# Optimization experiments

Measured on AMD Instinct MI355X. Metric: run time of the kernel, lower is better.

## Reference

```python
import jax, jax.numpy as jnp
import numpy as np

IN_FEATURES = 4096
OUT_FEATURES = 4096
MIN_PREC = 3   # min(precisions)
MAXMEM = 6
BL, BH = 4, 5  # floor/ceil of p = sigmoid(0)*3 + 3 = 4.5 (static, matches p.item() usage)


def dequant_kbit(qweight, lut, b):
    """Bitplane LUT dequant: qweight (P, O, IN//32) int32, lut (O, 2**b) -> (O, IN) float.
    Plane j holds one bit per weight (32 weights packed per int32, LSB-first within
    the int32); the first b planes form the b-bit code, plane 0 being the MSB."""
    planes = qweight[:b]                                   # (b, O, IN//32)
    shifts = jnp.arange(32, dtype=jnp.int32)               # bit position within int32
    bits = (planes[..., None] >> shifts) & 1               # (b, O, IN//32, 32)
    bits = bits.reshape(b, planes.shape[1], -1)            # (b, O, IN)
    weights = (jnp.arange(b, dtype=jnp.int32)[::-1])[:, None, None]  # MSB-first
    code = jnp.sum(bits << weights, axis=0)                # (O, IN) int32 in [0, 2**b)
    return jnp.take_along_axis(lut, code, axis=1)          # (O, IN)


def setup_inputs() -> dict:
    key = jax.random.key(0)
    k_x, k_q, k_l4, k_l5, k_b = jax.random.split(key, 5)
    x = jax.random.normal(k_x, (4, 2048, IN_FEATURES), dtype=jnp.float32)
    z = jnp.float32(0.0)  # z_inv = log(z_init/(1-z_init)) with z_init=0.5
    qweight = jax.random.randint(k_q, (MAXMEM, OUT_FEATURES, IN_FEATURES // 32),
                                 minval=-(2**31), maxval=2**31 - 1, dtype=jnp.int32)
    # LUTs: sorted quantization levels per output row (realistic for quantized linear)
    lut4 = jnp.sort(0.02 * jax.random.normal(k_l4, (OUT_FEATURES, 2**BL), dtype=jnp.float32), axis=-1)
    lut5 = jnp.sort(0.02 * jax.random.normal(k_l5, (OUT_FEATURES, 2**BH), dtype=jnp.float32), axis=-1)
    bias = 0.01 * jax.random.normal(k_b, (OUT_FEATURES,), dtype=jnp.float32)
    return {"x": x, "z": z, "lut4": lut4, "lut5": lut5, "bias": bias, "qweight": qweight}


def reference(x, z, lut4, lut5, bias, qweight):
    prange_len = MAXMEM - MIN_PREC
    p = jax.nn.sigmoid(z) * prange_len + MIN_PREC   # 4.5 at init
    r = 1.0 - (p - BL)                              # blend weight for low-bit branch
    wl = dequant_kbit(qweight, lut4, BL)            # (O, IN)
    wh = dequant_kbit(qweight, lut5, BH)            # (O, IN)
    yl = jnp.einsum('bsi,oi->bso', x, wl)
    yh = jnp.einsum('bsi,oi->bso', x, wh)
    return yl * r + yh * (1.0 - r) + bias
```

## Files before the change

kernel.cpp:

```cpp
#include <hip/hip_runtime.h>
#include <hip/hip_bf16.h>


#define IN_F   4096
#define OUT_F  4096
#define M_DIM  8192

#define CAST_BLOCKS 8192
#define DEQ_BLOCKS  2048

typedef __bf16          bf16x8   __attribute__((ext_vector_type(8)));
typedef float           f32x4    __attribute__((ext_vector_type(4)));
typedef unsigned short  ushortx8 __attribute__((ext_vector_type(8)));

__device__ __forceinline__ unsigned short f32_to_bf16(float f) {
    unsigned int u = __builtin_bit_cast(unsigned int, f);
    u += 0x7fffu + ((u >> 16) & 1u);
    return (unsigned short)(u >> 16);
}

__device__ __forceinline__ void async_load16(const void* g, void* l) {
    __builtin_amdgcn_global_load_lds(
        (const __attribute__((address_space(1))) unsigned int*)g,
        (__attribute__((address_space(3))) unsigned int*)l,
        16, 0, 0);
}

__global__ __launch_bounds__(256) void prologue_kernel(
    const float* __restrict__ x,
    const unsigned int* __restrict__ qw,
    const float* __restrict__ lut4,
    const float* __restrict__ lut5,
    const float* __restrict__ zp,
    unsigned short* __restrict__ xb,
    unsigned short* __restrict__ W)
{
    const int tid = threadIdx.x;

    if (blockIdx.x < CAST_BLOCKS) {
        const size_t i = (size_t)blockIdx.x * 4096 + (size_t)tid * 16;
        const f32x4* src = (const f32x4*)(x + i);
        f32x4 a0 = src[0], a1 = src[1], a2 = src[2], a3 = src[3];
        ushortx8 o0, o1;
        #pragma unroll
        for (int e = 0; e < 4; ++e) {
            o0[e]     = f32_to_bf16(a0[e]);
            o0[4 + e] = f32_to_bf16(a1[e]);
            o1[e]     = f32_to_bf16(a2[e]);
            o1[4 + e] = f32_to_bf16(a3[e]);
        }
        ushortx8* dst = (ushortx8*)(xb + i);
        dst[0] = o0;
        dst[1] = o1;
        return;
    }

    __shared__ float sc[2][32];
    const int bid = blockIdx.x - CAST_BLOCKS;
    const int o0 = bid * 2;

    if (tid < 64) {
        const float z   = zp[0];
        const float sig = 1.0f / (1.0f + __expf(-z));
        const float r   = 2.0f - 3.0f * sig;
        const float ri  = 1.0f - r;
        const int row = tid >> 5;
        const int c   = tid & 31;
        sc[row][c] = r * lut4[(o0 + row) * 16 + (c >> 1)]
                   + ri * lut5[(o0 + row) * 32 + c];
    }
    __syncthreads();

    const int gid = bid * 256 + tid;
    const int lo  = (gid >> 7) & 1;

    const int PS = OUT_F * (IN_F / 32);
    const unsigned int q0 = qw[0 * PS + gid];
    const unsigned int q1 = qw[1 * PS + gid];
    const unsigned int q2 = qw[2 * PS + gid];
    const unsigned int q3 = qw[3 * PS + gid];
    const unsigned int q4 = qw[4 * PS + gid];

    unsigned short outv[32];
    #pragma unroll
    for (int i = 0; i < 32; ++i) {
        const unsigned c5 = (((q0 >> i) & 1u) << 4) | (((q1 >> i) & 1u) << 3) |
                            (((q2 >> i) & 1u) << 2) | (((q3 >> i) & 1u) << 1) |
                             ((q4 >> i) & 1u);
        outv[i] = f32_to_bf16(sc[lo][c5]);
    }

    ushortx8* dst = (ushortx8*)(W + (size_t)gid * 32);
    #pragma unroll
    for (int j = 0; j < 4; ++j) {
        ushortx8 v;
        #pragma unroll
        for (int e = 0; e < 8; ++e) v[e] = outv[j * 8 + e];
        dst[j] = v;
    }
}

__global__ __launch_bounds__(256) void gemm_bt_kernel(
    const unsigned short* __restrict__ A,
    const unsigned short* __restrict__ B,
    const float* __restrict__ bias,
    float* __restrict__ C)
{
    __shared__ unsigned short sA[128 * 32];
    __shared__ unsigned short sB[128 * 32];

    const int tid  = threadIdx.x;
    const int lane = tid & 63;
    const int wave = tid >> 6;
    const int bn = blockIdx.x;
    const int bm = blockIdx.y;

    const int wm  = (wave & 1) << 6;
    const int wn  = (wave >> 1) << 6;
    const int l15 = lane & 15;
    const int q   = lane >> 4;

    const int e0 = tid * 8;
    const int r0 = e0 >> 5;
    const int c0 = e0 & 31;

    const unsigned short* gA0 = A + (size_t)(bm * 128 + r0) * IN_F + c0;
    const unsigned short* gA1 = gA0 + (size_t)64 * IN_F;
    const unsigned short* gB0 = B + (size_t)(bn * 128 + r0) * IN_F + c0;
    const unsigned short* gB1 = gB0 + (size_t)64 * IN_F;
    char* lA0 = (char*)sA + e0 * 2;
    char* lA1 = lA0 + 4096;
    char* lB0 = (char*)sB + e0 * 2;
    char* lB1 = lB0 + 4096;

    f32x4 acc[4][4] = {};

    const int aoff = (wm + l15) * 32 + q * 8;
    const int boff = (wn + l15) * 32 + q * 8;

    for (int k0 = 0; k0 < IN_F; k0 += 32) {
        async_load16(gA0 + k0, lA0);
        async_load16(gA1 + k0, lA1);
        async_load16(gB0 + k0, lB0);
        async_load16(gB1 + k0, lB1);
        __syncthreads();

        bf16x8 af[4], bf[4];
        #pragma unroll
        for (int mi = 0; mi < 4; ++mi)
            af[mi] = *(const bf16x8*)(sA + aoff + mi * 512);
        #pragma unroll
        for (int ni = 0; ni < 4; ++ni)
            bf[ni] = *(const bf16x8*)(sB + boff + ni * 512);

        #pragma unroll
        for (int mi = 0; mi < 4; ++mi)
            #pragma unroll
            for (int ni = 0; ni < 4; ++ni)
                acc[mi][ni] = __builtin_amdgcn_mfma_f32_16x16x32_bf16(
                    af[mi], bf[ni], acc[mi][ni], 0, 0, 0);

        __syncthreads();
    }

    const int col0 = bn * 128 + wn + l15;
    const int row0 = bm * 128 + wm + q * 4;
    #pragma unroll
    for (int ni = 0; ni < 4; ++ni) {
        const int col = col0 + ni * 16;
        const float bv = bias[col];
        #pragma unroll
        for (int mi = 0; mi < 4; ++mi) {
            const int row = row0 + mi * 16;
            #pragma unroll
            for (int r = 0; r < 4; ++r)
                C[(size_t)(row + r) * OUT_F + col] = acc[mi][ni][r] + bv;
        }
    }
}

extern "C" void kernel_launch(void* const* d_in, const int* in_sizes, int n_in,
                              void* d_out, int out_size, void* d_ws, size_t ws_size,
                              hipStream_t stream)
{
    const float*        x    = (const float*)d_in[0];
    const float*        z    = (const float*)d_in[1];
    const float*        lut4 = (const float*)d_in[2];
    const float*        lut5 = (const float*)d_in[3];
    const float*        bias = (const float*)d_in[4];
    const unsigned int* qw   = (const unsigned int*)d_in[5];
    float* out = (float*)d_out;

    unsigned short* xb = (unsigned short*)d_ws;
    unsigned short* wb = xb + (size_t)M_DIM * IN_F;

    prologue_kernel<<<CAST_BLOCKS + DEQ_BLOCKS, 256, 0, stream>>>(
        x, qw, lut4, lut5, z, xb, wb);
    gemm_bt_kernel<<<dim3(OUT_F / 128, M_DIM / 128), 256, 0, stream>>>(xb, wb, bias, out);
}
```

Baseline: 569.0 us.

## Rewrite bf16 GEMM with 256x256 tiles, double-buffered LDS pipeline and swizzle

The GEMM kernel now computes 256x256 output tiles with 512 threads and a K step of 64. A and B tiles are double-buffered in LDS and prefetched with global_load_lds in half-tile stages that overlap the MFMA phases, with explicit barriers, waitcnts and setprio. The LDS layout is XOR-swizzled to avoid bank conflicts, and the block index is remapped for L2 locality. This targets the previous kernel's single-buffered load-then-compute stalls and low reuse per tile, at the cost of 128KB of LDS, heavier register use (128 accumulators per thread), and fragile hand-written synchronization.

```diff
diff --git a/kernel.cpp b/kernel.cpp
--- a/kernel.cpp
+++ b/kernel.cpp
@@ -8,6 +8,8 @@
 
 #define CAST_BLOCKS 8192
 #define DEQ_BLOCKS  2048
+
+#define NT (IN_F / 64)
 
 typedef __bf16          bf16x8   __attribute__((ext_vector_type(8)));
 typedef float           f32x4    __attribute__((ext_vector_type(4)));
@@ -24,6 +26,12 @@
         (const __attribute__((address_space(1))) unsigned int*)g,
         (__attribute__((address_space(3))) unsigned int*)l,
         16, 0, 0);
+}
+
+__device__ __forceinline__ void stage_half(const unsigned short* g0,
+                                           unsigned short* l0) {
+    async_load16(g0, l0);
+    async_load16(g0 + (size_t)64 * IN_F, l0 + 4096);
 }
 
 __global__ __launch_bounds__(256) void prologue_kernel(
@@ -100,81 +108,163 @@
     }
 }
 
-__global__ __launch_bounds__(256) void gemm_bt_kernel(
+
+#define MFMA_BF16 __builtin_amdgcn_mfma_f32_16x16x32_bf16
+
+__device__ __forceinline__ void tile_step(
+    int t,
+    const unsigned short* cA, unsigned short* cB, unsigned short* nA,
+    int tid,
+    const unsigned short* gA0, const unsigned short* gA1,
+    const unsigned short* gB0, const unsigned short* gB1,
+    int aBase, int bBase, int ck0, int ck1,
+    f32x4 (&acc)[8][4])
+{
+    bf16x8 af[4], bf0[4], bf1[4];
+
+    #pragma unroll
+    for (int m = 0; m < 4; ++m)
+        af[m] = *(const bf16x8*)(cA + aBase + m * 1024 + ck0);
+    #pragma unroll
+    for (int n = 0; n < 4; ++n)
+        bf0[n] = *(const bf16x8*)(cB + bBase + n * 1024 + ck0);
+    if (t + 1 < NT) stage_half(gA0 + (size_t)(t + 1) * 64, nA + tid * 8);
+    __builtin_amdgcn_s_barrier();
+    asm volatile("s_waitcnt lgkmcnt(0)" ::: "memory");
+    __builtin_amdgcn_sched_barrier(0);
+    __builtin_amdgcn_s_setprio(1);
+    #pragma unroll
+    for (int m = 0; m < 4; ++m)
+        #pragma unroll
+        for (int n = 0; n < 4; ++n)
+            acc[m][n] = MFMA_BF16(af[m], bf0[n], acc[m][n], 0, 0, 0);
+    __builtin_amdgcn_s_setprio(0);
+    __builtin_amdgcn_sched_barrier(0);
+    __builtin_amdgcn_s_barrier();
+
+    #pragma unroll
+    for (int m = 0; m < 4; ++m)
+        af[m] = *(const bf16x8*)(cA + aBase + m * 1024 + ck1);
+    #pragma unroll
+    for (int n = 0; n < 4; ++n)
+        bf1[n] = *(const bf16x8*)(cB + bBase + n * 1024 + ck1);
+    if (t + 1 < NT) stage_half(gA1 + (size_t)(t + 1) * 64, nA + 8192 + tid * 8);
+    __builtin_amdgcn_s_barrier();
+    asm volatile("s_waitcnt lgkmcnt(0)" ::: "memory");
+    __builtin_amdgcn_sched_barrier(0);
+    __builtin_amdgcn_s_setprio(1);
+    #pragma unroll
+    for (int m = 0; m < 4; ++m)
+        #pragma unroll
+        for (int n = 0; n < 4; ++n)
+            acc[m][n] = MFMA_BF16(af[m], bf1[n], acc[m][n], 0, 0, 0);
+    __builtin_amdgcn_s_setprio(0);
+    __builtin_amdgcn_sched_barrier(0);
+    __builtin_amdgcn_s_barrier();
+
+    #pragma unroll
+    for (int m = 0; m < 4; ++m)
+        af[m] = *(const bf16x8*)(cA + aBase + (m + 4) * 1024 + ck0);
+    if (t + 2 < NT) stage_half(gB0 + (size_t)(t + 2) * 64, cB + tid * 8);
+    __builtin_amdgcn_s_barrier();
+    asm volatile("s_waitcnt lgkmcnt(0)" ::: "memory");
+    __builtin_amdgcn_sched_barrier(0);
+    __builtin_amdgcn_s_setprio(1);
+    #pragma unroll
+    for (int m = 0; m < 4; ++m)
+        #pragma unroll
+        for (int n = 0; n < 4; ++n)
+            acc[m + 4][n] = MFMA_BF16(af[m], bf0[n], acc[m + 4][n], 0, 0, 0);
+    __builtin_amdgcn_s_setprio(0);
+    __builtin_amdgcn_sched_barrier(0);
+    __builtin_amdgcn_s_barrier();
+
+    #pragma unroll
+    for (int m = 0; m < 4; ++m)
+        af[m] = *(const bf16x8*)(cA + aBase + (m + 4) * 1024 + ck1);
+    if (t + 2 < NT) stage_half(gB1 + (size_t)(t + 2) * 64, cB + 8192 + tid * 8);
+    if (t < NT - 2) asm volatile("s_waitcnt vmcnt(4)" ::: "memory");
+    else            asm volatile("s_waitcnt vmcnt(0)" ::: "memory");
+    __builtin_amdgcn_s_barrier();
+    asm volatile("s_waitcnt lgkmcnt(0)" ::: "memory");
+    __builtin_amdgcn_sched_barrier(0);
+    __builtin_amdgcn_s_setprio(1);
+    #pragma unroll
+    for (int m = 0; m < 4; ++m)
+        #pragma unroll
+        for (int n = 0; n < 4; ++n)
+            acc[m + 4][n] = MFMA_BF16(af[m], bf1[n], acc[m + 4][n], 0, 0, 0);
+    __builtin_amdgcn_s_setprio(0);
+    __builtin_amdgcn_sched_barrier(0);
+    __builtin_amdgcn_s_barrier();
+}
+
+__global__ __launch_bounds__(512, 2) void gemm_bt_kernel(
     const unsigned short* __restrict__ A,
     const unsigned short* __restrict__ B,
     const float* __restrict__ bias,
     float* __restrict__ C)
 {
-    __shared__ unsigned short sA[128 * 32];
-    __shared__ unsigned short sB[128 * 32];
-
-    const int tid  = threadIdx.x;
-    const int lane = tid & 63;
-    const int wave = tid >> 6;
-    const int bn = blockIdx.x;
-    const int bm = blockIdx.y;
-
-    const int wm  = (wave & 1) << 6;
-    const int wn  = (wave >> 1) << 6;
-    const int l15 = lane & 15;
-    const int q   = lane >> 4;
-
-    const int e0 = tid * 8;
-    const int r0 = e0 >> 5;
-    const int c0 = e0 & 31;
-
-    const unsigned short* gA0 = A + (size_t)(bm * 128 + r0) * IN_F + c0;
-    const unsigned short* gA1 = gA0 + (size_t)64 * IN_F;
-    const unsigned short* gB0 = B + (size_t)(bn * 128 + r0) * IN_F + c0;
-    const unsigned short* gB1 = gB0 + (size_t)64 * IN_F;
-    char* lA0 = (char*)sA + e0 * 2;
-    char* lA1 = lA0 + 4096;
-    char* lB0 = (char*)sB + e0 * 2;
-    char* lB1 = lB0 + 4096;
-
-    f32x4 acc[4][4] = {};
-
-    const int aoff = (wm + l15) * 32 + q * 8;
-    const int boff = (wn + l15) * 32 + q * 8;
-
-    for (int k0 = 0; k0 < IN_F; k0 += 32) {
-        async_load16(gA0 + k0, lA0);
-        async_load16(gA1 + k0, lA1);
-        async_load16(gB0 + k0, lB0);
-        async_load16(gB1 + k0, lB1);
-        __syncthreads();
-
-        bf16x8 af[4], bf[4];
-        #pragma unroll
-        for (int mi = 0; mi < 4; ++mi)
-            af[mi] = *(const bf16x8*)(sA + aoff + mi * 512);
-        #pragma unroll
-        for (int ni = 0; ni < 4; ++ni)
-            bf[ni] = *(const bf16x8*)(sB + boff + ni * 512);
-
-        #pragma unroll
-        for (int mi = 0; mi < 4; ++mi)
+    __shared__ unsigned short sA[2][256 * 64];
+    __shared__ unsigned short sB[2][256 * 64];
+
+    const int tid = threadIdx.x;
+
+    const int id  = blockIdx.x;
+    const int swz = (id & 7) * 64 + (id >> 3);
+    const int bn  = swz & 15;
+    const int bm  = swz >> 4;
+
+    const int l   = tid & 63;
+    const int wv  = tid >> 6;
+    const int wr  = wv >> 2;
+    const int wc  = wv & 3;
+    const int l15 = l & 15;
+    const int q   = l >> 4;
+    const int xm  = l15 & 7;
+
+    const int aBase = (wr * 128 + l15) * 64;
+    const int bBase = (wc * 64  + l15) * 64;
+    const int ck0   = ((q)     ^ xm) * 8;
+    const int ck1   = ((4 + q) ^ xm) * 8;
+
+    const int r  = tid >> 3;
+    const int cx = ((tid & 7) ^ (r & 7)) * 8;
+    const unsigned short* gA0 = A + (size_t)(bm * 256 + r) * IN_F + cx;
+    const unsigned short* gA1 = gA0 + (size_t)128 * IN_F;
+    const unsigned short* gB0 = B + (size_t)(bn * 256 + r) * IN_F + cx;
+    const unsigned short* gB1 = gB0 + (size_t)128 * IN_F;
+
+    stage_half(gB0,      &sB[0][0] + tid * 8);
+    stage_half(gB1,      &sB[0][0] + 8192 + tid * 8);
+    stage_half(gA0,      &sA[0][0] + tid * 8);
+    stage_half(gA1,      &sA[0][0] + 8192 + tid * 8);
+    stage_half(gB0 + 64, &sB[1][0] + tid * 8);
+    stage_half(gB1 + 64, &sB[1][0] + 8192 + tid * 8);
+    asm volatile("s_waitcnt vmcnt(4)" ::: "memory");
+    __builtin_amdgcn_s_barrier();
+
+    f32x4 acc[8][4] = {};
+
+    #pragma unroll 1
+    for (int tp = 0; tp < NT; tp += 2) {
+        tile_step(tp,     &sA[0][0], &sB[0][0], &sA[1][0], tid,
+                  gA0, gA1, gB0, gB1, aBase, bBase, ck0, ck1, acc);
+        tile_step(tp + 1, &sA[1][0], &sB[1][0], &sA[0][0], tid,
+                  gA0, gA1, gB0, gB1, aBase, bBase, ck0, ck1, acc);
+    }
+
+    const int row0 = bm * 256 + wr * 128 + q * 4;
+    const int col0 = bn * 256 + wc * 64 + l15;
+    #pragma unroll
+    for (int n = 0; n < 4; ++n) {
+        const float bv = bias[col0 + n * 16];
+        #pragma unroll
+        for (int m = 0; m < 8; ++m) {
             #pragma unroll
-            for (int ni = 0; ni < 4; ++ni)
-                acc[mi][ni] = __builtin_amdgcn_mfma_f32_16x16x32_bf16(
-                    af[mi], bf[ni], acc[mi][ni], 0, 0, 0);
-
-        __syncthreads();
-    }
-
-    const int col0 = bn * 128 + wn + l15;
-    const int row0 = bm * 128 + wm + q * 4;
-    #pragma unroll
-    for (int ni = 0; ni < 4; ++ni) {
-        const int col = col0 + ni * 16;
-        const float bv = bias[col];
-        #pragma unroll
-        for (int mi = 0; mi < 4; ++mi) {
-            const int row = row0 + mi * 16;
-            #pragma unroll
-            for (int r = 0; r < 4; ++r)
-                C[(size_t)(row + r) * OUT_F + col] = acc[mi][ni][r] + bv;
+            for (int rr = 0; rr < 4; ++rr)
+                C[(size_t)(row0 + m * 16 + rr) * OUT_F + (col0 + n * 16)] =
+                    acc[m][n][rr] + bv;
         }
     }
 }
@@ -196,5 +286,6 @@
 
     prologue_kernel<<<CAST_BLOCKS + DEQ_BLOCKS, 256, 0, stream>>>(
         x, qw, lut4, lut5, z, xb, wb);
-    gemm_bt_kernel<<<dim3(OUT_F / 128, M_DIM / 128), 256, 0, stream>>>(xb, wb, bias, out);
-}
+    gemm_bt_kernel<<<(M_DIM / 256) * (OUT_F / 256), 512, 0, stream>>>(
+        xb, wb, bias, out);
+}
```

After: 481.7 us. -15.4%, faster.
